# Optimization experiments

Measured on AMD Instinct MI355X. Metric: run time of the kernel, lower is better.

Reference implementation:

```python
import jax, jax.numpy as jnp
import numpy as np

B, F, DU, DI, DT = 4096, 50, 128, 256, 768
NU, NI = 200000, 100000
EPS = 1e-5

def _batchnorm(x, gamma, beta):
    # training-mode BatchNorm1d: biased batch statistics
    mu = jnp.mean(x, axis=0)
    var = jnp.mean((x - mu) ** 2, axis=0)
    return gamma * (x - mu) / jnp.sqrt(var + EPS) + beta

def setup_inputs() -> dict:
    key = jax.random.key(0)
    ks = jax.random.split(key, 16)
    inp = {
        "user_id": jax.random.randint(ks[0], (B,), 0, NU),
        "item_id": jax.random.randint(ks[1], (B,), 0, NI),
        "user_follow": jax.random.randint(ks[2], (B, F), 0, NU),
        "follow_len": jax.random.randint(ks[3], (B,), 0, F + 1),
        "feature_item": jax.random.normal(ks[4], (B, 3), dtype=jnp.float32),
        "tag_emb": jax.random.normal(ks[5], (B, DT), dtype=jnp.float32),
        "user_emb_table": jax.random.normal(ks[6], (NU, DU), dtype=jnp.float32) * 0.02,
        "item_emb_table": jax.random.normal(ks[7], (NI, DI), dtype=jnp.float32) * 0.02,
        "fc1_w": jax.random.normal(ks[8], (DI, DT + DI), dtype=jnp.float32) * 0.02,
        "fc1_b": jnp.zeros((DI,), dtype=jnp.float32),
        "fc2_w": jax.random.normal(ks[9], (DU, DU + DI), dtype=jnp.float32) * 0.02,
        "fc2_b": jnp.zeros((DU,), dtype=jnp.float32),
        "out_w": jax.random.normal(ks[10], (1, DU + 3), dtype=jnp.float32) * 0.02,
        "out_b": jnp.zeros((1,), dtype=jnp.float32),
        "bn1_g": jnp.ones((DI,), dtype=jnp.float32),
        "bn1_b": jnp.zeros((DI,), dtype=jnp.float32),
        "bn2_g": jnp.ones((DU,), dtype=jnp.float32),
        "bn2_b": jnp.zeros((DU,), dtype=jnp.float32),
    }
    return inp

def reference(user_id, item_id, user_follow, follow_len, feature_item, tag_emb,
              user_emb_table, item_emb_table, fc1_w, fc1_b, fc2_w, fc2_b,
              out_w, out_b, bn1_g, bn1_b, bn2_g, bn2_b):
    # --- user interaction embedding (vectorized padded attention) ---
    u = user_emb_table[user_id]                       # [B, 128]
    f = user_emb_table[user_follow]                   # [B, F, 128]
    uf = jnp.concatenate([u[:, None, :], f], axis=1)  # [B, 1+F, 128]
    scores = jnp.einsum('bnd,bd->bn', uf, u)          # [B, 1+F]
    pos_valid = jnp.arange(F)[None, :] < follow_len[:, None]
    valid = jnp.concatenate([jnp.ones((user_id.shape[0], 1), dtype=bool), pos_valid], axis=1)
    scores = jnp.where(valid, scores, -1e9)
    w = jax.nn.softmax(scores, axis=1)
    att = jnp.einsum('bn,bnd->bd', w, uf)             # [B, 128]
    user_embedded = jnp.where((follow_len > 1)[:, None], att, u)
    # --- item fusion path ---
    item_embedded = item_emb_table[item_id]           # [B, 256]
    h1 = jnp.concatenate([tag_emb, item_embedded], axis=1) @ fc1_w.T + fc1_b
    item_vector = jax.nn.relu(_batchnorm(h1 + item_embedded, bn1_g, bn1_b))
    h2 = jnp.concatenate([user_embedded, item_vector], axis=1) @ fc2_w.T + fc2_b
    item_user_vector = jax.nn.relu(_batchnorm(h2 + user_embedded, bn2_g, bn2_b))
    logits = jnp.concatenate([item_user_vector, feature_item], axis=1) @ out_w.T + out_b
    return logits
```

## Files before the change

kernel.cpp:

```cpp
#include <hip/hip_runtime.h>
#include <cstdint>
#include <cstddef>

#define BATCH 4096
#define F_FOLLOW 50
#define NROW 51
#define DU 128
#define DI 256
#define DT 768
#define K1 (DT + DI)
#define K2 (DU + DI)
#define EPS 1e-5f

typedef float f32x4 __attribute__((ext_vector_type(4)));
typedef short s16x8 __attribute__((ext_vector_type(8)));

#define MFMA16(a, b, c) __builtin_amdgcn_mfma_f32_16x16x32_bf16(a, b, c, 0, 0, 0)

__device__ __forceinline__ unsigned rne16(float r) {
    unsigned b = __float_as_uint(r);
    return (b + 0x7FFFu + ((b >> 16) & 1u)) >> 16;
}
__device__ __forceinline__ void cvt4(float4 v, unsigned &h0, unsigned &h1,
                                     unsigned &l0, unsigned &l1) {
    unsigned bx = __float_as_uint(v.x), by = __float_as_uint(v.y);
    unsigned bz = __float_as_uint(v.z), bw = __float_as_uint(v.w);
    h0 = (bx >> 16) | (by & 0xFFFF0000u);
    h1 = (bz >> 16) | (bw & 0xFFFF0000u);
    float rx = v.x - __uint_as_float(bx & 0xFFFF0000u);
    float ry = v.y - __uint_as_float(by & 0xFFFF0000u);
    float rz = v.z - __uint_as_float(bz & 0xFFFF0000u);
    float rw = v.w - __uint_as_float(bw & 0xFFFF0000u);
    l0 = rne16(rx) | (rne16(ry) << 16);
    l1 = rne16(rz) | (rne16(rw) << 16);
}

__global__ __launch_bounds__(256) void attn_kernel(
    const int* __restrict__ user_id,
    const int* __restrict__ user_follow,
    const int* __restrict__ follow_len,
    const float* __restrict__ utab,
    float* __restrict__ uemb_out,
    float* __restrict__ zero_region)
{
    __shared__ float uf[NROW * 133];
    __shared__ int   idx[NROW];
    __shared__ float w[NROW];
    __shared__ float sArr[64];
    __shared__ float pacc[256];

    const int b   = blockIdx.x;
    const int tid = threadIdx.x;

    if (b == 0)
        for (int i = tid; i < 768; i += 256) zero_region[i] = 0.f;

    const int fl = follow_len[b];
    const int nv = fl < F_FOLLOW ? fl : F_FOLLOW;

    if (tid < NROW)
        idx[tid] = (tid == 0) ? user_id[b] : user_follow[b * F_FOLLOW + tid - 1];
    __syncthreads();

    const int nrows = nv + 1;
    for (int e = tid; e < nrows * 32; e += 256) {
        int n = e >> 5, d4 = (e & 31) << 2;
        float4 v = *(const float4*)(utab + (size_t)idx[n] * 128 + d4);
        float* dst = &uf[n * 133 + d4];
        dst[0] = v.x; dst[1] = v.y; dst[2] = v.z; dst[3] = v.w;
    }
    __syncthreads();

    {
        int n = tid >> 2, q = tid & 3;
        float acc = 0.f;
        if (n <= nv) {
            int d0 = q * 32;
            #pragma unroll 8
            for (int dd = 0; dd < 32; ++dd) {
                int d = d0 + ((dd + q * 8) & 31);
                acc += uf[n * 133 + d] * uf[d];
            }
        }
        acc += __shfl_xor(acc, 1);
        acc += __shfl_xor(acc, 2);
        if (q == 0 && n <= nv) sArr[n] = acc;
    }
    __syncthreads();

    if (tid < 64) {
        float s = (tid <= nv) ? sArr[tid] : -1e30f;
        float m = s;
        #pragma unroll
        for (int off = 32; off; off >>= 1)
            m = fmaxf(m, __shfl_xor(m, off, 64));
        float e = expf(s - m);
        float l = e;
        #pragma unroll
        for (int off = 32; off; off >>= 1)
            l += __shfl_xor(l, off, 64);
        if (tid <= nv) w[tid] = e / l;
    }
    __syncthreads();

    {
        int d = tid & 127, half = tid >> 7;
        float o = 0.f;
        for (int n = half; n <= nv; n += 2)
            o += w[n] * uf[n * 133 + d];
        pacc[tid] = o;
    }
    __syncthreads();
    if (tid < 128) {
        float o = pacc[tid] + pacc[tid + 128];
        float outv = (fl > 1) ? o : uf[tid];
        uemb_out[(size_t)b * DU + tid] = outv;
    }
}

__global__ __launch_bounds__(256) void gemm1_kernel(
    const float* __restrict__ tag,
    const int*   __restrict__ item_id,
    const float* __restrict__ itab,
    const float* __restrict__ w1,
    const float* __restrict__ b1,
    float* __restrict__ a1,
    float* __restrict__ gsum,
    float* __restrict__ gsq)
{
    __shared__ __align__(16) unsigned short Ah[64][40], Al[64][40];
    __shared__ __align__(16) unsigned short Bh[64][40], Bl[64][40];
    __shared__ int   iid[64];
    __shared__ float lsum[64], lsq[64];

    const int tid = threadIdx.x;
    const int m0 = blockIdx.x * 64;
    const int n0 = blockIdx.y * 64;

    if (tid < 64) { iid[tid] = item_id[m0 + tid]; lsum[tid] = 0.f; lsq[tid] = 0.f; }

    const int r  = tid >> 2;
    const int k8 = (tid & 3) * 8;

    const int w  = tid >> 6;
    const int l  = tid & 63;
    const int wr = (w >> 1) * 32;
    const int wc = (w & 1) * 32;
    const int fr = l & 15;
    const int fk = (l >> 4) * 8;

    f32x4 acc00 = {}, acc01 = {}, acc10 = {}, acc11 = {};

    float4 ra0, ra1, rb0, rb1;
    {
        const float* ap = tag + (size_t)(m0 + r) * DT + k8;
        ra0 = *(const float4*)ap;  ra1 = *(const float4*)(ap + 4);
        const float* bp = w1 + (size_t)(n0 + r) * K1 + k8;
        rb0 = *(const float4*)bp;  rb1 = *(const float4*)(bp + 4);
    }
    __syncthreads();

    for (int kt = 0; kt < K1; kt += 32) {
        if (kt) __syncthreads();

        unsigned h0, h1, h2, h3, l0, l1, l2, l3;
        cvt4(ra0, h0, h1, l0, l1); cvt4(ra1, h2, h3, l2, l3);
        *(uint4*)&Ah[r][k8] = make_uint4(h0, h1, h2, h3);
        *(uint4*)&Al[r][k8] = make_uint4(l0, l1, l2, l3);
        cvt4(rb0, h0, h1, l0, l1); cvt4(rb1, h2, h3, l2, l3);
        *(uint4*)&Bh[r][k8] = make_uint4(h0, h1, h2, h3);
        *(uint4*)&Bl[r][k8] = make_uint4(l0, l1, l2, l3);

        if (kt + 32 < K1) {
            const int kn = kt + 32;
            const float* ap;
            if (kn < DT) ap = tag + (size_t)(m0 + r) * DT + kn + k8;
            else         ap = itab + (size_t)iid[r] * DI + (kn - DT) + k8;
            ra0 = *(const float4*)ap;  ra1 = *(const float4*)(ap + 4);
            const float* bp = w1 + (size_t)(n0 + r) * K1 + kn + k8;
            rb0 = *(const float4*)bp;  rb1 = *(const float4*)(bp + 4);
        }
        __syncthreads();

        s16x8 ah0 = *(const s16x8*)&Ah[wr + fr][fk];
        s16x8 ah1 = *(const s16x8*)&Ah[wr + 16 + fr][fk];
        s16x8 al0 = *(const s16x8*)&Al[wr + fr][fk];
        s16x8 al1 = *(const s16x8*)&Al[wr + 16 + fr][fk];
        s16x8 bh0 = *(const s16x8*)&Bh[wc + fr][fk];
        s16x8 bh1 = *(const s16x8*)&Bh[wc + 16 + fr][fk];
        s16x8 bl0 = *(const s16x8*)&Bl[wc + fr][fk];
        s16x8 bl1 = *(const s16x8*)&Bl[wc + 16 + fr][fk];

        acc00 = MFMA16(ah0, bh0, acc00);
        acc01 = MFMA16(ah0, bh1, acc01);
        acc10 = MFMA16(ah1, bh0, acc10);
        acc11 = MFMA16(ah1, bh1, acc11);
        acc00 = MFMA16(ah0, bl0, acc00);
        acc01 = MFMA16(ah0, bl1, acc01);
        acc10 = MFMA16(ah1, bl0, acc10);
        acc11 = MFMA16(ah1, bl1, acc11);
        acc00 = MFMA16(al0, bh0, acc00);
        acc01 = MFMA16(al0, bh1, acc01);
        acc10 = MFMA16(al1, bh0, acc10);
        acc11 = MFMA16(al1, bh1, acc11);
    }

    const f32x4 accs[2][2] = {{acc00, acc01}, {acc10, acc11}};
    #pragma unroll
    for (int ct = 0; ct < 2; ++ct) {
        int cg  = wc + ct * 16 + fr;
        int col = n0 + cg;
        float bias = b1[col];
        float s_ = 0.f, q_ = 0.f;
        #pragma unroll
        for (int rt = 0; rt < 2; ++rt) {
            int rb = wr + rt * 16 + ((l >> 4) << 2);
            #pragma unroll
            for (int i = 0; i < 4; ++i) {
                int rl = rb + i;
                float v = accs[rt][ct][i] + bias + itab[(size_t)iid[rl] * DI + col];
                a1[(size_t)(m0 + rl) * DI + col] = v;
                s_ += v; q_ += v * v;
            }
        }
        s_ += __shfl_xor(s_, 16); s_ += __shfl_xor(s_, 32);
        q_ += __shfl_xor(q_, 16); q_ += __shfl_xor(q_, 32);
        if (l < 16) { atomicAdd(&lsum[cg], s_); atomicAdd(&lsq[cg], q_); }
    }
    __syncthreads();
    if (tid < 64) {
        atomicAdd(&gsum[n0 + tid], lsum[tid]);
        atomicAdd(&gsq [n0 + tid], lsq [tid]);
    }
}

__global__ __launch_bounds__(256) void gemm2_kernel(
    const float* __restrict__ uemb,
    const float* __restrict__ a1,
    const float* __restrict__ gsum1,
    const float* __restrict__ gsq1,
    const float* __restrict__ g1,
    const float* __restrict__ bb1,
    const float* __restrict__ w2,
    const float* __restrict__ b2,
    float* __restrict__ a2,
    float* __restrict__ gsum,
    float* __restrict__ gsq)
{
    __shared__ __align__(16) unsigned short Ah[64][40], Al[64][40];
    __shared__ __align__(16) unsigned short Bh[64][40], Bl[64][40];
    __shared__ __align__(16) float sc1s[256], sh1s[256];
    __shared__ float lsum[64], lsq[64];

    const int tid = threadIdx.x;
    const int m0 = blockIdx.x * 64;
    const int n0 = blockIdx.y * 64;

    {
        float mean = gsum1[tid] * (1.f / 4096.f);
        float var  = gsq1[tid] * (1.f / 4096.f) - mean * mean;
        var = fmaxf(var, 0.f);
        float sc = g1[tid] / sqrtf(var + EPS);
        sc1s[tid] = sc;
        sh1s[tid] = bb1[tid] - mean * sc;
    }
    if (tid < 64) { lsum[tid] = 0.f; lsq[tid] = 0.f; }

    const int r  = tid >> 2;
    const int k8 = (tid & 3) * 8;
    const int w  = tid >> 6;
    const int l  = tid & 63;
    const int wr = (w >> 1) * 32;
    const int wc = (w & 1) * 32;
    const int fr = l & 15;
    const int fk = (l >> 4) * 8;

    f32x4 acc00 = {}, acc01 = {}, acc10 = {}, acc11 = {};

    float4 ra0, ra1, rb0, rb1;
    {
        const float* ap = uemb + (size_t)(m0 + r) * DU + k8;
        ra0 = *(const float4*)ap;  ra1 = *(const float4*)(ap + 4);
        const float* bp = w2 + (size_t)(n0 + r) * K2 + k8;
        rb0 = *(const float4*)bp;  rb1 = *(const float4*)(bp + 4);
    }
    __syncthreads();

    for (int kt = 0; kt < K2; kt += 32) {
        if (kt) __syncthreads();

        unsigned h0, h1, h2, h3, l0, l1, l2, l3;
        cvt4(ra0, h0, h1, l0, l1); cvt4(ra1, h2, h3, l2, l3);
        *(uint4*)&Ah[r][k8] = make_uint4(h0, h1, h2, h3);
        *(uint4*)&Al[r][k8] = make_uint4(l0, l1, l2, l3);
        cvt4(rb0, h0, h1, l0, l1); cvt4(rb1, h2, h3, l2, l3);
        *(uint4*)&Bh[r][k8] = make_uint4(h0, h1, h2, h3);
        *(uint4*)&Bl[r][k8] = make_uint4(l0, l1, l2, l3);

        if (kt + 32 < K2) {
            const int kn = kt + 32;
            if (kn < DU) {
                const float* ap = uemb + (size_t)(m0 + r) * DU + kn + k8;
                ra0 = *(const float4*)ap;  ra1 = *(const float4*)(ap + 4);
            } else {
                int c = kn + k8 - DU;
                float4 v0 = *(const float4*)(a1 + (size_t)(m0 + r) * DI + c);
                float4 v1 = *(const float4*)(a1 + (size_t)(m0 + r) * DI + c + 4);
                float4 s0 = *(const float4*)&sc1s[c];
                float4 s1 = *(const float4*)&sc1s[c + 4];
                float4 h0v = *(const float4*)&sh1s[c];
                float4 h1v = *(const float4*)&sh1s[c + 4];
                ra0.x = fmaxf(v0.x * s0.x + h0v.x, 0.f);
                ra0.y = fmaxf(v0.y * s0.y + h0v.y, 0.f);
                ra0.z = fmaxf(v0.z * s0.z + h0v.z, 0.f);
                ra0.w = fmaxf(v0.w * s0.w + h0v.w, 0.f);
                ra1.x = fmaxf(v1.x * s1.x + h1v.x, 0.f);
                ra1.y = fmaxf(v1.y * s1.y + h1v.y, 0.f);
                ra1.z = fmaxf(v1.z * s1.z + h1v.z, 0.f);
                ra1.w = fmaxf(v1.w * s1.w + h1v.w, 0.f);
            }
            const float* bp = w2 + (size_t)(n0 + r) * K2 + kn + k8;
            rb0 = *(const float4*)bp;  rb1 = *(const float4*)(bp + 4);
        }
        __syncthreads();

        s16x8 ah0 = *(const s16x8*)&Ah[wr + fr][fk];
        s16x8 ah1 = *(const s16x8*)&Ah[wr + 16 + fr][fk];
        s16x8 al0 = *(const s16x8*)&Al[wr + fr][fk];
        s16x8 al1 = *(const s16x8*)&Al[wr + 16 + fr][fk];
        s16x8 bh0 = *(const s16x8*)&Bh[wc + fr][fk];
        s16x8 bh1 = *(const s16x8*)&Bh[wc + 16 + fr][fk];
        s16x8 bl0 = *(const s16x8*)&Bl[wc + fr][fk];
        s16x8 bl1 = *(const s16x8*)&Bl[wc + 16 + fr][fk];

        acc00 = MFMA16(ah0, bh0, acc00);
        acc01 = MFMA16(ah0, bh1, acc01);
        acc10 = MFMA16(ah1, bh0, acc10);
        acc11 = MFMA16(ah1, bh1, acc11);
        acc00 = MFMA16(ah0, bl0, acc00);
        acc01 = MFMA16(ah0, bl1, acc01);
        acc10 = MFMA16(ah1, bl0, acc10);
        acc11 = MFMA16(ah1, bl1, acc11);
        acc00 = MFMA16(al0, bh0, acc00);
        acc01 = MFMA16(al0, bh1, acc01);
        acc10 = MFMA16(al1, bh0, acc10);
        acc11 = MFMA16(al1, bh1, acc11);
    }

    const f32x4 accs[2][2] = {{acc00, acc01}, {acc10, acc11}};
    #pragma unroll
    for (int ct = 0; ct < 2; ++ct) {
        int cg  = wc + ct * 16 + fr;
        int col = n0 + cg;
        float bias = b2[col];
        float s_ = 0.f, q_ = 0.f;
        #pragma unroll
        for (int rt = 0; rt < 2; ++rt) {
            int rb = wr + rt * 16 + ((l >> 4) << 2);
            #pragma unroll
            for (int i = 0; i < 4; ++i) {
                int rl = rb + i;
                float v = accs[rt][ct][i] + bias + uemb[(size_t)(m0 + rl) * DU + col];
                a2[(size_t)(m0 + rl) * DU + col] = v;
                s_ += v; q_ += v * v;
            }
        }
        s_ += __shfl_xor(s_, 16); s_ += __shfl_xor(s_, 32);
        q_ += __shfl_xor(q_, 16); q_ += __shfl_xor(q_, 32);
        if (l < 16) { atomicAdd(&lsum[cg], s_); atomicAdd(&lsq[cg], q_); }
    }
    __syncthreads();
    if (tid < 64) {
        atomicAdd(&gsum[n0 + tid], lsum[tid]);
        atomicAdd(&gsq [n0 + tid], lsq [tid]);
    }
}

__global__ __launch_bounds__(256) void final_kernel(
    const float* __restrict__ a2,
    const float* __restrict__ gsum2,
    const float* __restrict__ gsq2,
    const float* __restrict__ g2,
    const float* __restrict__ bb2,
    const float* __restrict__ feat,
    const float* __restrict__ ow, const float* __restrict__ ob,
    float* __restrict__ out)
{
    __shared__ float sc2s[128];
    __shared__ float sh2s[128];

    const int tid  = threadIdx.x;
    if (tid < 128) {
        float mean = gsum2[tid] * (1.f / 4096.f);
        float var  = gsq2[tid] * (1.f / 4096.f) - mean * mean;
        var = fmaxf(var, 0.f);
        float sc = g2[tid] / sqrtf(var + EPS);
        sc2s[tid] = sc;
        sh2s[tid] = bb2[tid] - mean * sc;
    }
    __syncthreads();

    const int lane = tid & 63;
    const int wv   = tid >> 6;
    const int b    = blockIdx.x * 4 + wv;

    float acc = 0.f;
    #pragma unroll
    for (int h = 0; h < 2; ++h) {
        int j = lane + h * 64;
        float v = fmaxf(a2[(size_t)b * DU + j] * sc2s[j] + sh2s[j], 0.f);
        acc += v * ow[j];
    }
    #pragma unroll
    for (int off = 32; off; off >>= 1)
        acc += __shfl_xor(acc, off, 64);
    if (lane == 0) {
        acc += feat[(size_t)b * 3 + 0] * ow[128]
             + feat[(size_t)b * 3 + 1] * ow[129]
             + feat[(size_t)b * 3 + 2] * ow[130]
             + ob[0];
        out[b] = acc;
    }
}

extern "C" void kernel_launch(void* const* d_in, const int* in_sizes, int n_in,
                              void* d_out, int out_size, void* d_ws, size_t ws_size,
                              hipStream_t stream)
{
    const int*   user_id = (const int*)d_in[0];
    const int*   item_id = (const int*)d_in[1];
    const int*   ufollow = (const int*)d_in[2];
    const int*   flen    = (const int*)d_in[3];
    const float* feat    = (const float*)d_in[4];
    const float* tag     = (const float*)d_in[5];
    const float* utab    = (const float*)d_in[6];
    const float* itab    = (const float*)d_in[7];
    const float* w1      = (const float*)d_in[8];
    const float* b1      = (const float*)d_in[9];
    const float* w2      = (const float*)d_in[10];
    const float* b2      = (const float*)d_in[11];
    const float* ow      = (const float*)d_in[12];
    const float* ob      = (const float*)d_in[13];
    const float* g1      = (const float*)d_in[14];
    const float* bb1     = (const float*)d_in[15];
    const float* g2      = (const float*)d_in[16];
    const float* bb2     = (const float*)d_in[17];

    float* ws     = (float*)d_ws;
    float* uemb   = ws;
    float* a1     = uemb + BATCH * DU;
    float* a2     = a1 + BATCH * DI;
    float* sum1   = a2 + BATCH * DU;
    float* sumsq1 = sum1 + 256;
    float* sum2   = sumsq1 + 256;
    float* sumsq2 = sum2 + 128;

    attn_kernel<<<BATCH, 256, 0, stream>>>(user_id, ufollow, flen, utab, uemb,
                                           sum1);
    gemm1_kernel<<<dim3(64, 4), 256, 0, stream>>>(tag, item_id, itab, w1, b1, a1,
                                                  sum1, sumsq1);
    gemm2_kernel<<<dim3(64, 2), 256, 0, stream>>>(uemb, a1, sum1, sumsq1, g1, bb1,
                                                  w2, b2, a2, sum2, sumsq2);
    final_kernel<<<1024, 256, 0, stream>>>(a2, sum2, sumsq2, g2, bb2, feat, ow, ob,
                                           (float*)d_out);
}
```

Before: 283.0 us.

## Fuse attention and GEMM1 into one launch, replace atomics with partial-sum buffers

```diff
diff --git a/kernel.cpp b/kernel.cpp
--- a/kernel.cpp
+++ b/kernel.cpp
@@ -35,217 +35,217 @@
     l1 = rne16(rz) | (rne16(rw) << 16);
 }
 
-__global__ __launch_bounds__(256) void attn_kernel(
+struct AttnSmem {
+    float uf[NROW * 133];
+    int   idx[NROW];
+    float w[NROW];
+    float sArr[64];
+    float pacc[256];
+};
+struct Gemm1Smem {
+    unsigned short Ah[64][40], Al[64][40], Bh[64][40], Bl[64][40];
+    int   iid[64];
+    float lsum[64], lsq[64];
+};
+union __align__(16) FusedSmem { AttnSmem a; Gemm1Smem g; };
+
+__global__ __launch_bounds__(256) void fused_attn_gemm1(
     const int* __restrict__ user_id,
     const int* __restrict__ user_follow,
     const int* __restrict__ follow_len,
     const float* __restrict__ utab,
-    float* __restrict__ uemb_out,
-    float* __restrict__ zero_region)
-{
-    __shared__ float uf[NROW * 133];
-    __shared__ int   idx[NROW];
-    __shared__ float w[NROW];
-    __shared__ float sArr[64];
-    __shared__ float pacc[256];
-
-    const int b   = blockIdx.x;
-    const int tid = threadIdx.x;
-
-    if (b == 0)
-        for (int i = tid; i < 768; i += 256) zero_region[i] = 0.f;
-
-    const int fl = follow_len[b];
-    const int nv = fl < F_FOLLOW ? fl : F_FOLLOW;
-
-    if (tid < NROW)
-        idx[tid] = (tid == 0) ? user_id[b] : user_follow[b * F_FOLLOW + tid - 1];
-    __syncthreads();
-
-    const int nrows = nv + 1;
-    for (int e = tid; e < nrows * 32; e += 256) {
-        int n = e >> 5, d4 = (e & 31) << 2;
-        float4 v = *(const float4*)(utab + (size_t)idx[n] * 128 + d4);
-        float* dst = &uf[n * 133 + d4];
-        dst[0] = v.x; dst[1] = v.y; dst[2] = v.z; dst[3] = v.w;
-    }
-    __syncthreads();
-
-    {
-        int n = tid >> 2, q = tid & 3;
-        float acc = 0.f;
-        if (n <= nv) {
-            int d0 = q * 32;
-            #pragma unroll 8
-            for (int dd = 0; dd < 32; ++dd) {
-                int d = d0 + ((dd + q * 8) & 31);
-                acc += uf[n * 133 + d] * uf[d];
-            }
-        }
-        acc += __shfl_xor(acc, 1);
-        acc += __shfl_xor(acc, 2);
-        if (q == 0 && n <= nv) sArr[n] = acc;
-    }
-    __syncthreads();
-
-    if (tid < 64) {
-        float s = (tid <= nv) ? sArr[tid] : -1e30f;
-        float m = s;
-        #pragma unroll
-        for (int off = 32; off; off >>= 1)
-            m = fmaxf(m, __shfl_xor(m, off, 64));
-        float e = expf(s - m);
-        float l = e;
-        #pragma unroll
-        for (int off = 32; off; off >>= 1)
-            l += __shfl_xor(l, off, 64);
-        if (tid <= nv) w[tid] = e / l;
-    }
-    __syncthreads();
-
-    {
-        int d = tid & 127, half = tid >> 7;
-        float o = 0.f;
-        for (int n = half; n <= nv; n += 2)
-            o += w[n] * uf[n * 133 + d];
-        pacc[tid] = o;
-    }
-    __syncthreads();
-    if (tid < 128) {
-        float o = pacc[tid] + pacc[tid + 128];
-        float outv = (fl > 1) ? o : uf[tid];
-        uemb_out[(size_t)b * DU + tid] = outv;
-    }
-}
-
-__global__ __launch_bounds__(256) void gemm1_kernel(
     const float* __restrict__ tag,
     const int*   __restrict__ item_id,
     const float* __restrict__ itab,
     const float* __restrict__ w1,
     const float* __restrict__ b1,
+    float* __restrict__ uemb_out,
     float* __restrict__ a1,
-    float* __restrict__ gsum,
-    float* __restrict__ gsq)
+    float* __restrict__ part1s,
+    float* __restrict__ part1q)
 {
-    __shared__ __align__(16) unsigned short Ah[64][40], Al[64][40];
-    __shared__ __align__(16) unsigned short Bh[64][40], Bl[64][40];
-    __shared__ int   iid[64];
-    __shared__ float lsum[64], lsq[64];
-
+    __shared__ FusedSmem sm;
     const int tid = threadIdx.x;
-    const int m0 = blockIdx.x * 64;
-    const int n0 = blockIdx.y * 64;
-
-    if (tid < 64) { iid[tid] = item_id[m0 + tid]; lsum[tid] = 0.f; lsq[tid] = 0.f; }
-
-    const int r  = tid >> 2;
-    const int k8 = (tid & 3) * 8;
-
-    const int w  = tid >> 6;
-    const int l  = tid & 63;
-    const int wr = (w >> 1) * 32;
-    const int wc = (w & 1) * 32;
-    const int fr = l & 15;
-    const int fk = (l >> 4) * 8;
-
-    f32x4 acc00 = {}, acc01 = {}, acc10 = {}, acc11 = {};
-
-    float4 ra0, ra1, rb0, rb1;
-    {
-        const float* ap = tag + (size_t)(m0 + r) * DT + k8;
-        ra0 = *(const float4*)ap;  ra1 = *(const float4*)(ap + 4);
-        const float* bp = w1 + (size_t)(n0 + r) * K1 + k8;
-        rb0 = *(const float4*)bp;  rb1 = *(const float4*)(bp + 4);
-    }
-    __syncthreads();
-
-    for (int kt = 0; kt < K1; kt += 32) {
-        if (kt) __syncthreads();
-
-        unsigned h0, h1, h2, h3, l0, l1, l2, l3;
-        cvt4(ra0, h0, h1, l0, l1); cvt4(ra1, h2, h3, l2, l3);
-        *(uint4*)&Ah[r][k8] = make_uint4(h0, h1, h2, h3);
-        *(uint4*)&Al[r][k8] = make_uint4(l0, l1, l2, l3);
-        cvt4(rb0, h0, h1, l0, l1); cvt4(rb1, h2, h3, l2, l3);
-        *(uint4*)&Bh[r][k8] = make_uint4(h0, h1, h2, h3);
-        *(uint4*)&Bl[r][k8] = make_uint4(l0, l1, l2, l3);
-
-        if (kt + 32 < K1) {
-            const int kn = kt + 32;
-            const float* ap;
-            if (kn < DT) ap = tag + (size_t)(m0 + r) * DT + kn + k8;
-            else         ap = itab + (size_t)iid[r] * DI + (kn - DT) + k8;
+
+    if (blockIdx.x < 256) {
+        auto& G = sm.g;
+        const int bm = blockIdx.x >> 2;
+        const int m0 = bm * 64;
+        const int n0 = (blockIdx.x & 3) * 64;
+
+        if (tid < 64) { G.iid[tid] = item_id[m0 + tid]; G.lsum[tid] = 0.f; G.lsq[tid] = 0.f; }
+
+        const int r  = tid >> 2;
+        const int k8 = (tid & 3) * 8;
+        const int w  = tid >> 6;
+        const int l  = tid & 63;
+        const int wr = (w >> 1) * 32;
+        const int wc = (w & 1) * 32;
+        const int fr = l & 15;
+        const int fk = (l >> 4) * 8;
+
+        f32x4 acc00 = {}, acc01 = {}, acc10 = {}, acc11 = {};
+
+        float4 ra0, ra1, rb0, rb1;
+        {
+            const float* ap = tag + (size_t)(m0 + r) * DT + k8;
             ra0 = *(const float4*)ap;  ra1 = *(const float4*)(ap + 4);
-            const float* bp = w1 + (size_t)(n0 + r) * K1 + kn + k8;
+            const float* bp = w1 + (size_t)(n0 + r) * K1 + k8;
             rb0 = *(const float4*)bp;  rb1 = *(const float4*)(bp + 4);
         }
         __syncthreads();
 
-        s16x8 ah0 = *(const s16x8*)&Ah[wr + fr][fk];
-        s16x8 ah1 = *(const s16x8*)&Ah[wr + 16 + fr][fk];
-        s16x8 al0 = *(const s16x8*)&Al[wr + fr][fk];
-        s16x8 al1 = *(const s16x8*)&Al[wr + 16 + fr][fk];
-        s16x8 bh0 = *(const s16x8*)&Bh[wc + fr][fk];
-        s16x8 bh1 = *(const s16x8*)&Bh[wc + 16 + fr][fk];
-        s16x8 bl0 = *(const s16x8*)&Bl[wc + fr][fk];
-        s16x8 bl1 = *(const s16x8*)&Bl[wc + 16 + fr][fk];
-
-        acc00 = MFMA16(ah0, bh0, acc00);
-        acc01 = MFMA16(ah0, bh1, acc01);
-        acc10 = MFMA16(ah1, bh0, acc10);
-        acc11 = MFMA16(ah1, bh1, acc11);
-        acc00 = MFMA16(ah0, bl0, acc00);
-        acc01 = MFMA16(ah0, bl1, acc01);
-        acc10 = MFMA16(ah1, bl0, acc10);
-        acc11 = MFMA16(ah1, bl1, acc11);
-        acc00 = MFMA16(al0, bh0, acc00);
-        acc01 = MFMA16(al0, bh1, acc01);
-        acc10 = MFMA16(al1, bh0, acc10);
-        acc11 = MFMA16(al1, bh1, acc11);
-    }
-
-    const f32x4 accs[2][2] = {{acc00, acc01}, {acc10, acc11}};
-    #pragma unroll
-    for (int ct = 0; ct < 2; ++ct) {
-        int cg  = wc + ct * 16 + fr;
-        int col = n0 + cg;
-        float bias = b1[col];
-        float s_ = 0.f, q_ = 0.f;
-        #pragma unroll
-        for (int rt = 0; rt < 2; ++rt) {
-            int rb = wr + rt * 16 + ((l >> 4) << 2);
+        for (int kt = 0; kt < K1; kt += 32) {
+            if (kt) __syncthreads();
+
+            unsigned h0, h1, h2, h3, l0, l1, l2, l3;
+            cvt4(ra0, h0, h1, l0, l1); cvt4(ra1, h2, h3, l2, l3);
+            *(uint4*)&G.Ah[r][k8] = make_uint4(h0, h1, h2, h3);
+            *(uint4*)&G.Al[r][k8] = make_uint4(l0, l1, l2, l3);
+            cvt4(rb0, h0, h1, l0, l1); cvt4(rb1, h2, h3, l2, l3);
+            *(uint4*)&G.Bh[r][k8] = make_uint4(h0, h1, h2, h3);
+            *(uint4*)&G.Bl[r][k8] = make_uint4(l0, l1, l2, l3);
+
+            if (kt + 32 < K1) {
+                const int kn = kt + 32;
+                const float* ap;
+                if (kn < DT) ap = tag + (size_t)(m0 + r) * DT + kn + k8;
+                else         ap = itab + (size_t)G.iid[r] * DI + (kn - DT) + k8;
+                ra0 = *(const float4*)ap;  ra1 = *(const float4*)(ap + 4);
+                const float* bp = w1 + (size_t)(n0 + r) * K1 + kn + k8;
+                rb0 = *(const float4*)bp;  rb1 = *(const float4*)(bp + 4);
+            }
+            __syncthreads();
+
+            s16x8 ah0 = *(const s16x8*)&G.Ah[wr + fr][fk];
+            s16x8 ah1 = *(const s16x8*)&G.Ah[wr + 16 + fr][fk];
+            s16x8 al0 = *(const s16x8*)&G.Al[wr + fr][fk];
+            s16x8 al1 = *(const s16x8*)&G.Al[wr + 16 + fr][fk];
+            s16x8 bh0 = *(const s16x8*)&G.Bh[wc + fr][fk];
+            s16x8 bh1 = *(const s16x8*)&G.Bh[wc + 16 + fr][fk];
+            s16x8 bl0 = *(const s16x8*)&G.Bl[wc + fr][fk];
+            s16x8 bl1 = *(const s16x8*)&G.Bl[wc + 16 + fr][fk];
+
+            acc00 = MFMA16(ah0, bh0, acc00);
+            acc01 = MFMA16(ah0, bh1, acc01);
+            acc10 = MFMA16(ah1, bh0, acc10);
+            acc11 = MFMA16(ah1, bh1, acc11);
+            acc00 = MFMA16(ah0, bl0, acc00);
+            acc01 = MFMA16(ah0, bl1, acc01);
+            acc10 = MFMA16(ah1, bl0, acc10);
+            acc11 = MFMA16(ah1, bl1, acc11);
+            acc00 = MFMA16(al0, bh0, acc00);
+            acc01 = MFMA16(al0, bh1, acc01);
+            acc10 = MFMA16(al1, bh0, acc10);
+            acc11 = MFMA16(al1, bh1, acc11);
+        }
+
+        const f32x4 accs[2][2] = {{acc00, acc01}, {acc10, acc11}};
+        #pragma unroll
+        for (int ct = 0; ct < 2; ++ct) {
+            int cg  = wc + ct * 16 + fr;
+            int col = n0 + cg;
+            float bias = b1[col];
+            float s_ = 0.f, q_ = 0.f;
             #pragma unroll
-            for (int i = 0; i < 4; ++i) {
-                int rl = rb + i;
-                float v = accs[rt][ct][i] + bias + itab[(size_t)iid[rl] * DI + col];
-                a1[(size_t)(m0 + rl) * DI + col] = v;
-                s_ += v; q_ += v * v;
+            for (int rt = 0; rt < 2; ++rt) {
+                int rb = wr + rt * 16 + ((l >> 4) << 2);
+                #pragma unroll
+                for (int i = 0; i < 4; ++i) {
+                    int rl = rb + i;
+                    float v = accs[rt][ct][i] + bias + itab[(size_t)G.iid[rl] * DI + col];
+                    a1[(size_t)(m0 + rl) * DI + col] = v;
+                    s_ += v; q_ += v * v;
+                }
             }
-        }
-        s_ += __shfl_xor(s_, 16); s_ += __shfl_xor(s_, 32);
-        q_ += __shfl_xor(q_, 16); q_ += __shfl_xor(q_, 32);
-        if (l < 16) { atomicAdd(&lsum[cg], s_); atomicAdd(&lsq[cg], q_); }
-    }
-    __syncthreads();
-    if (tid < 64) {
-        atomicAdd(&gsum[n0 + tid], lsum[tid]);
-        atomicAdd(&gsq [n0 + tid], lsq [tid]);
+            s_ += __shfl_xor(s_, 16); s_ += __shfl_xor(s_, 32);
+            q_ += __shfl_xor(q_, 16); q_ += __shfl_xor(q_, 32);
+            if (l < 16) { atomicAdd(&G.lsum[cg], s_); atomicAdd(&G.lsq[cg], q_); }
+        }
+        __syncthreads();
+        if (tid < 64) {
+            part1s[(size_t)(n0 + tid) * 64 + bm] = G.lsum[tid];
+            part1q[(size_t)(n0 + tid) * 64 + bm] = G.lsq[tid];
+        }
+    } else {
+        auto& A = sm.a;
+        const int b  = blockIdx.x - 256;
+        const int fl = follow_len[b];
+        const int nv = fl < F_FOLLOW ? fl : F_FOLLOW;
+
+        if (tid < NROW)
+            A.idx[tid] = (tid == 0) ? user_id[b] : user_follow[b * F_FOLLOW + tid - 1];
+        __syncthreads();
+
+        const int nrows = nv + 1;
+        for (int e = tid; e < nrows * 32; e += 256) {
+            int n = e >> 5, d4 = (e & 31) << 2;
+            float4 v = *(const float4*)(utab + (size_t)A.idx[n] * 128 + d4);
+            float* dst = &A.uf[n * 133 + d4];
+            dst[0] = v.x; dst[1] = v.y; dst[2] = v.z; dst[3] = v.w;
+        }
+        __syncthreads();
+
+        {
+            int n = tid >> 2, q = tid & 3;
+            float acc = 0.f;
+            if (n <= nv) {
+                int d0 = q * 32;
+                #pragma unroll 8
+                for (int dd = 0; dd < 32; ++dd) {
+                    int d = d0 + ((dd + q * 8) & 31);
+                    acc += A.uf[n * 133 + d] * A.uf[d];
+                }
+            }
+            acc += __shfl_xor(acc, 1);
+            acc += __shfl_xor(acc, 2);
+            if (q == 0 && n <= nv) A.sArr[n] = acc;
+        }
+        __syncthreads();
+
+        if (tid < 64) {
+            float s = (tid <= nv) ? A.sArr[tid] : -1e30f;
+            float m = s;
+            #pragma unroll
+            for (int off = 32; off; off >>= 1)
+                m = fmaxf(m, __shfl_xor(m, off, 64));
+            float e = expf(s - m);
+            float l2 = e;
+            #pragma unroll
+            for (int off = 32; off; off >>= 1)
+                l2 += __shfl_xor(l2, off, 64);
+            if (tid <= nv) A.w[tid] = e / l2;
+        }
+        __syncthreads();
+
+        {
+            int d = tid & 127, half = tid >> 7;
+            float o = 0.f;
+            for (int n = half; n <= nv; n += 2)
+                o += A.w[n] * A.uf[n * 133 + d];
+            A.pacc[tid] = o;
+        }
+        __syncthreads();
+        if (tid < 128) {
+            float o = A.pacc[tid] + A.pacc[tid + 128];
+            float outv = (fl > 1) ? o : A.uf[tid];
+            uemb_out[(size_t)b * DU + tid] = outv;
+        }
     }
 }
 
 __global__ __launch_bounds__(256) void gemm2_kernel(
     const float* __restrict__ uemb,
     const float* __restrict__ a1,
-    const float* __restrict__ gsum1,
-    const float* __restrict__ gsq1,
+    const float* __restrict__ part1s,
+    const float* __restrict__ part1q,
     const float* __restrict__ g1,
     const float* __restrict__ bb1,
     const float* __restrict__ w2,
     const float* __restrict__ b2,
     float* __restrict__ a2,
-    float* __restrict__ gsum,
-    float* __restrict__ gsq)
+    float* __restrict__ part2s,
+    float* __restrict__ part2q)
 {
     __shared__ __align__(16) unsigned short Ah[64][40], Al[64][40];
     __shared__ __align__(16) unsigned short Bh[64][40], Bl[64][40];
@@ -253,13 +253,21 @@
     __shared__ float lsum[64], lsq[64];
 
     const int tid = threadIdx.x;
-    const int m0 = blockIdx.x * 64;
+    const int bm = blockIdx.x;
+    const int m0 = bm * 64;
     const int n0 = blockIdx.y * 64;
 
     {
-        float mean = gsum1[tid] * (1.f / 4096.f);
-        float var  = gsq1[tid] * (1.f / 4096.f) - mean * mean;
-        var = fmaxf(var, 0.f);
+        const float4* ps = (const float4*)(part1s + (size_t)tid * 64);
+        const float4* pq = (const float4*)(part1q + (size_t)tid * 64);
+        float s = 0.f, q = 0.f;
+        #pragma unroll
+        for (int j = 0; j < 16; ++j) {
+            float4 v = ps[j]; s += v.x + v.y + v.z + v.w;
+            float4 u = pq[j]; q += u.x + u.y + u.z + u.w;
+        }
+        float mean = s * (1.f / 4096.f);
+        float var  = fmaxf(q * (1.f / 4096.f) - mean * mean, 0.f);
         float sc = g1[tid] / sqrtf(var + EPS);
         sc1s[tid] = sc;
         sh1s[tid] = bb1[tid] - mean * sc;
@@ -371,15 +379,15 @@
     }
     __syncthreads();
     if (tid < 64) {
-        atomicAdd(&gsum[n0 + tid], lsum[tid]);
-        atomicAdd(&gsq [n0 + tid], lsq [tid]);
+        part2s[(size_t)(n0 + tid) * 64 + bm] = lsum[tid];
+        part2q[(size_t)(n0 + tid) * 64 + bm] = lsq[tid];
     }
 }
 
 __global__ __launch_bounds__(256) void final_kernel(
     const float* __restrict__ a2,
-    const float* __restrict__ gsum2,
-    const float* __restrict__ gsq2,
+    const float* __restrict__ part2s,
+    const float* __restrict__ part2q,
     const float* __restrict__ g2,
     const float* __restrict__ bb2,
     const float* __restrict__ feat,
@@ -389,11 +397,18 @@
     __shared__ float sc2s[128];
     __shared__ float sh2s[128];
 
-    const int tid  = threadIdx.x;
+    const int tid = threadIdx.x;
     if (tid < 128) {
-        float mean = gsum2[tid] * (1.f / 4096.f);
-        float var  = gsq2[tid] * (1.f / 4096.f) - mean * mean;
-        var = fmaxf(var, 0.f);
+        const float4* ps = (const float4*)(part2s + (size_t)tid * 64);
+        const float4* pq = (const float4*)(part2q + (size_t)tid * 64);
+        float s = 0.f, q = 0.f;
+        #pragma unroll
+        for (int j = 0; j < 16; ++j) {
+            float4 v = ps[j]; s += v.x + v.y + v.z + v.w;
+            float4 u = pq[j]; q += u.x + u.y + u.z + u.w;
+        }
+        float mean = s * (1.f / 4096.f);
+        float var  = fmaxf(q * (1.f / 4096.f) - mean * mean, 0.f);
         float sc = g2[tid] / sqrtf(var + EPS);
         sc2s[tid] = sc;
         sh2s[tid] = bb2[tid] - mean * sc;
@@ -402,24 +417,27 @@
 
     const int lane = tid & 63;
     const int wv   = tid >> 6;
-    const int b    = blockIdx.x * 4 + wv;
-
-    float acc = 0.f;
+
     #pragma unroll
-    for (int h = 0; h < 2; ++h) {
-        int j = lane + h * 64;
-        float v = fmaxf(a2[(size_t)b * DU + j] * sc2s[j] + sh2s[j], 0.f);
-        acc += v * ow[j];
-    }
-    #pragma unroll
-    for (int off = 32; off; off >>= 1)
-        acc += __shfl_xor(acc, off, 64);
-    if (lane == 0) {
-        acc += feat[(size_t)b * 3 + 0] * ow[128]
-             + feat[(size_t)b * 3 + 1] * ow[129]
-             + feat[(size_t)b * 3 + 2] * ow[130]
-             + ob[0];
-        out[b] = acc;
+    for (int rr = 0; rr < 4; ++rr) {
+        const int b = blockIdx.x * 16 + wv * 4 + rr;
+        float acc = 0.f;
+        #pragma unroll
+        for (int h = 0; h < 2; ++h) {
+            int j = lane + h * 64;
+            float v = fmaxf(a2[(size_t)b * DU + j] * sc2s[j] + sh2s[j], 0.f);
+            acc += v * ow[j];
+        }
+        #pragma unroll
+        for (int off = 32; off; off >>= 1)
+            acc += __shfl_xor(acc, off, 64);
+        if (lane == 0) {
+            acc += feat[(size_t)b * 3 + 0] * ow[128]
+                 + feat[(size_t)b * 3 + 1] * ow[129]
+                 + feat[(size_t)b * 3 + 2] * ow[130]
+                 + ob[0];
+            out[b] = acc;
+        }
     }
 }
 
@@ -450,17 +468,16 @@
     float* uemb   = ws;
     float* a1     = uemb + BATCH * DU;
     float* a2     = a1 + BATCH * DI;
-    float* sum1   = a2 + BATCH * DU;
-    float* sumsq1 = sum1 + 256;
-    float* sum2   = sumsq1 + 256;
-    float* sumsq2 = sum2 + 128;
-
-    attn_kernel<<<BATCH, 256, 0, stream>>>(user_id, ufollow, flen, utab, uemb,
-                                           sum1);
-    gemm1_kernel<<<dim3(64, 4), 256, 0, stream>>>(tag, item_id, itab, w1, b1, a1,
-                                                  sum1, sumsq1);
-    gemm2_kernel<<<dim3(64, 2), 256, 0, stream>>>(uemb, a1, sum1, sumsq1, g1, bb1,
-                                                  w2, b2, a2, sum2, sumsq2);
-    final_kernel<<<1024, 256, 0, stream>>>(a2, sum2, sumsq2, g2, bb2, feat, ow, ob,
-                                           (float*)d_out);
-}
+    float* part1s = a2 + BATCH * DU;
+    float* part1q = part1s + 256 * 64;
+    float* part2s = part1q + 256 * 64;
+    float* part2q = part2s + 128 * 64;
+
+    fused_attn_gemm1<<<4352, 256, 0, stream>>>(user_id, ufollow, flen, utab,
+                                               tag, item_id, itab, w1, b1,
+                                               uemb, a1, part1s, part1q);
+    gemm2_kernel<<<dim3(64, 2), 256, 0, stream>>>(uemb, a1, part1s, part1q, g1, bb1,
+                                                  w2, b2, a2, part2s, part2q);
+    final_kernel<<<256, 256, 0, stream>>>(a2, part2s, part2q, g2, bb2, feat, ow, ob,
+                                          (float*)d_out);
+}
```

Measured after the change: 267.7 us. -5.4%, faster.
